# Optimization experiments

Measured on AMD Instinct MI355X. Metric: run time of the kernel, lower is better.

Reference implementation:

```python
import jax, jax.numpy as jnp
import numpy as np

B = 8
N_GENES = 19836
D_IN = 11
D_H = 64
DEG = 16
N = B * N_GENES
E_PER = N_GENES * DEG


def setup_inputs() -> dict:
    key = jax.random.key(0)
    ks = jax.random.split(key, 20)
    x = jax.random.normal(ks[0], (B, N_GENES, D_IN), dtype=jnp.float32)
    # edges: random within each graph, offset by graph index
    base_src = jax.random.randint(ks[1], (B, E_PER), 0, N_GENES)
    base_dst = jax.random.randint(ks[2], (B, E_PER), 0, N_GENES)
    offs = (jnp.arange(B) * N_GENES)[:, None]
    src = (base_src + offs).reshape(-1).astype(jnp.int64) if False else (base_src + offs).reshape(-1)
    dst = (base_dst + offs).reshape(-1)
    s = 0.02
    def nrm(k, shape):
        return jax.random.normal(k, shape, dtype=jnp.float32) * s
    return {
        'x': x, 'src': src, 'dst': dst,
        'enc_W': nrm(ks[3], (D_H, D_IN)), 'enc_b': jnp.zeros((D_H,), jnp.float32),
        'gene_emb': nrm(ks[4], (N_GENES, D_H)),
        'gin_W': nrm(ks[5], (D_H, D_H)),
        'bn_w': 1.0 + nrm(ks[6], (D_H,)), 'bn_b': jnp.zeros((D_H,), jnp.float32),
        'key_W': nrm(ks[7], (D_H, D_H)), 'key_b': jnp.zeros((D_H,), jnp.float32),
        'query_w': nrm(ks[8], (1, D_H)),
        'val_W': nrm(ks[9], (D_H, D_H)), 'val_b': jnp.zeros((D_H,), jnp.float32),
        'sae_enc_W': nrm(ks[10], (D_H, D_H)), 'sae_enc_b': jnp.zeros((D_H,), jnp.float32),
        'sae_dec_W': nrm(ks[11], (D_H, D_H)), 'sae_dec_b': jnp.zeros((D_H,), jnp.float32),
        'pred_W1': nrm(ks[12], (D_H, D_H)), 'pred_b1': jnp.zeros((D_H,), jnp.float32),
        'pred_W2': nrm(ks[13], (1, D_H)), 'pred_b2': jnp.zeros((1,), jnp.float32),
    }


def gelu(x):
    return jax.nn.gelu(x, approximate=False)  # nn.GELU default = exact erf


def batchnorm(h, w, b, eps=1e-5):
    # training-mode BatchNorm1d: batch statistics, biased variance
    mu = jnp.mean(h, axis=0)
    var = jnp.mean((h - mu) ** 2, axis=0)
    return (h - mu) * jax.lax.rsqrt(var + eps) * w + b


def reference(x, src, dst, enc_W, enc_b, gene_emb, gin_W, bn_w, bn_b,
              key_W, key_b, query_w, val_W, val_b,
              sae_enc_W, sae_enc_b, sae_dec_W, sae_dec_b,
              pred_W1, pred_b1, pred_W2, pred_b2):
    bsz, n_gene, d_in = x.shape
    n_nodes = bsz * n_gene
    # gene encoder: single Linear (bias) + GELU (inner batchnorm result is discarded in source)
    h = gelu(x.reshape(-1, d_in) @ enc_W.T + enc_b)          # [N, D_H]
    h = (h.reshape(bsz, n_gene, -1) + gene_emb).reshape(n_nodes, -1)
    # GIN layer (eps=0, sum aggregation): MLP(h + sum_{u->v} h_u); MLP = single Linear, no bias
    agg = jax.ops.segment_sum(h[src], dst, num_segments=n_nodes)  # irregular gather/scatter
    h = (h + agg) @ gin_W.T
    h = gelu(batchnorm(h, bn_w, bn_b))
    # attentive readout with SAE
    keys = h @ key_W.T + key_b
    w = jax.nn.sigmoid(keys @ query_w.T)                     # [N, 1]
    v = h @ val_W.T + val_b
    z = v * w
    enc = jax.nn.relu(z @ sae_enc_W.T + sae_enc_b)
    dec = enc @ sae_dec_W.T + sae_dec_b
    sae_loss = jnp.mean((dec - z) ** 2) + 1.0 * jnp.mean(jnp.abs(enc))
    gid = jnp.arange(n_nodes) // n_gene
    g_h = jax.ops.segment_sum(dec * w, gid, num_segments=bsz)  # [B, D_H]
    # predictor: Linear+GELU, Linear (inner batchnorm discarded in source)
    preds = gelu(g_h @ pred_W1.T + pred_b1) @ pred_W2.T + pred_b2
    return preds, w, sae_loss, dec
```

## Files before the change

kernel.cpp:

```cpp
#include <hip/hip_runtime.h>
#include <math.h>

#define NGENES 19836
#define BATCH 8
#define DIN 11
#define DH 64
#define NNODES (BATCH * NGENES)
#define NEDGES (NNODES * 16)
#define NDH (NNODES * DH)
#define NWAVE ((NNODES + 63) / 64)
#define NBLK_NODE ((NWAVE + 3) / 4)

#define SCAN_CHUNK 1024
#define NSBLK ((NNODES + SCAN_CHUNK - 1) / SCAN_CHUNK)

#define OUT_PREDS 0
#define OUT_W 8
#define OUT_SAE (8 + NNODES)
#define OUT_DEC (9 + NNODES)

__device__ __forceinline__ float gelu_f(float x) {
    return 0.5f * x * (1.0f + erff(x * 0.70710678118654752f));
}

__device__ __forceinline__ float bcast(float v, int lane) {
    return __int_as_float(__builtin_amdgcn_readlane(__float_as_int(v), lane));
}

__device__ __forceinline__ float wave_sum(float v) {
    #pragma unroll
    for (int o = 32; o; o >>= 1) v += __shfl_xor(v, o, 64);
    return v;
}

__global__ void k_encoder(const float* __restrict__ x, const float* __restrict__ encW,
                          const float* __restrict__ encB, const float* __restrict__ gemb,
                          float* __restrict__ h) {
    int lane = threadIdx.x & 63;
    int wid = (blockIdx.x * blockDim.x + threadIdx.x) >> 6;
    int tw = (gridDim.x * blockDim.x) >> 6;
    int chunk = (NNODES + tw - 1) / tw;
    int start = wid * chunk;
    int end = min(start + chunk, NNODES);
    float wreg[DIN];
    #pragma unroll
    for (int k = 0; k < DIN; ++k) wreg[k] = encW[lane * DIN + k];
    float bias = encB[lane];
    for (int node = start; node < end; ++node) {
        const float* xr = x + (size_t)node * DIN;
        float acc = bias;
        #pragma unroll
        for (int k = 0; k < DIN; ++k) acc = fmaf(xr[k], wreg[k], acc);
        int gene = node % NGENES;
        h[(size_t)node * DH + lane] = gelu_f(acc) + gemb[(size_t)gene * DH + lane];
    }
}

__global__ void k_hist(const int* __restrict__ dst, int* __restrict__ counts) {
    int i = blockIdx.x * blockDim.x + threadIdx.x;
    int stride = gridDim.x * blockDim.x;
    for (int e = i; e < NEDGES; e += stride)
        atomicAdd(&counts[dst[e]], 1);
}

__global__ void k_scan1(const int* __restrict__ counts, int* __restrict__ bsum) {
    __shared__ int red[256];
    int base = blockIdx.x * SCAN_CHUNK + threadIdx.x * 4;
    int s = 0;
    #pragma unroll
    for (int i = 0; i < 4; ++i) {
        int n = base + i;
        if (n < NNODES) s += counts[n];
    }
    red[threadIdx.x] = s;
    __syncthreads();
    for (int o = 128; o; o >>= 1) {
        if (threadIdx.x < o) red[threadIdx.x] += red[threadIdx.x + o];
        __syncthreads();
    }
    if (threadIdx.x == 0) bsum[blockIdx.x] = red[0];
}

__global__ void k_scan2(const int* __restrict__ bsum, int* __restrict__ boff) {
    __shared__ int red[256];
    int t = threadIdx.x;
    int v = (t < NSBLK) ? bsum[t] : 0;
    red[t] = v;
    __syncthreads();
    for (int o = 1; o < 256; o <<= 1) {
        int u = (t >= o) ? red[t - o] : 0;
        __syncthreads();
        red[t] += u;
        __syncthreads();
    }
    if (t < NSBLK) boff[t] = red[t] - v;
}

__global__ void k_scan3(const int* __restrict__ counts, const int* __restrict__ boff,
                        int* __restrict__ offsets, int* __restrict__ cursor) {
    __shared__ int red[256];
    int t = threadIdx.x;
    int base = blockIdx.x * SCAN_CHUNK + t * 4;
    int c[4];
    int s = 0;
    #pragma unroll
    for (int i = 0; i < 4; ++i) {
        int n = base + i;
        c[i] = (n < NNODES) ? counts[n] : 0;
        s += c[i];
    }
    red[t] = s;
    __syncthreads();
    for (int o = 1; o < 256; o <<= 1) {
        int v = (t >= o) ? red[t - o] : 0;
        __syncthreads();
        red[t] += v;
        __syncthreads();
    }
    int excl = red[t] - s + boff[blockIdx.x];
    #pragma unroll
    for (int i = 0; i < 4; ++i) {
        int n = base + i;
        if (n < NNODES) { offsets[n] = excl; cursor[n] = excl; }
        excl += c[i];
    }
}

__global__ void k_scatter(const int* __restrict__ src, const int* __restrict__ dst,
                          int* __restrict__ cursor, unsigned short* __restrict__ csr) {
    int i = blockIdx.x * blockDim.x + threadIdx.x;
    int stride = gridDim.x * blockDim.x;
    for (int e = i; e < NEDGES; e += stride) {
        int p = atomicAdd(&cursor[dst[e]], 1);
        csr[p] = (unsigned short)(src[e] % NGENES);
    }
}

__global__ void __launch_bounds__(256, 3)
k_aggin(const float* __restrict__ h, const int* __restrict__ offsets,
        const int* __restrict__ counts, const unsigned short* __restrict__ csr,
        const float* __restrict__ ginW, float* __restrict__ h2,
        float* __restrict__ stats) {
    int lane = threadIdx.x & 63;
    int wid = (blockIdx.x * blockDim.x + threadIdx.x) >> 6;
    int tw = (gridDim.x * blockDim.x) >> 6;
    float wr[DH];
    #pragma unroll
    for (int k = 0; k < DH; ++k) wr[k] = ginW[lane * DH + k];
    float s1 = 0.f, s2 = 0.f;
    for (int node = wid; node < NNODES; node += tw) {
        int gbase = (node / NGENES) * NGENES;
        float a[8];
        a[0] = h[(size_t)node * DH + lane];
        #pragma unroll
        for (int i = 1; i < 8; ++i) a[i] = 0.f;
        int start = offsets[node];
        int cnt = counts[node];
        for (int e0 = 0; e0 < cnt; e0 += 64) {
            int nn = min(64, cnt - e0);
            int iv = (lane < nn) ? (int)csr[start + e0 + lane] : 0;
            int j = 0;
            for (; j + 7 < nn; j += 8) {
                #pragma unroll
                for (int u = 0; u < 8; ++u) {
                    int v = gbase + __shfl(iv, j + u, 64);
                    a[u] += h[(size_t)v * DH + lane];
                }
            }
            for (; j < nn; ++j)
                a[0] += h[(size_t)(gbase + __shfl(iv, j, 64)) * DH + lane];
        }
        float tval = ((a[0] + a[1]) + (a[2] + a[3])) + ((a[4] + a[5]) + (a[6] + a[7]));
        float m0 = 0.f, m1 = 0.f, m2 = 0.f, m3 = 0.f;
        #pragma unroll
        for (int k = 0; k < DH; k += 4) {
            m0 = fmaf(wr[k], bcast(tval, k), m0);
            m1 = fmaf(wr[k + 1], bcast(tval, k + 1), m1);
            m2 = fmaf(wr[k + 2], bcast(tval, k + 2), m2);
            m3 = fmaf(wr[k + 3], bcast(tval, k + 3), m3);
        }
        float outv = (m0 + m1) + (m2 + m3);
        h2[(size_t)node * DH + lane] = outv;
        s1 += outv;
        s2 += outv * outv;
    }
    __shared__ float red[2][256];
    red[0][threadIdx.x] = s1;
    red[1][threadIdx.x] = s2;
    __syncthreads();
    if (threadIdx.x < 64) {
        float t1 = red[0][threadIdx.x] + red[0][threadIdx.x + 64] + red[0][threadIdx.x + 128] + red[0][threadIdx.x + 192];
        float t2 = red[1][threadIdx.x] + red[1][threadIdx.x + 64] + red[1][threadIdx.x + 128] + red[1][threadIdx.x + 192];
        atomicAdd(&stats[threadIdx.x], t1);
        atomicAdd(&stats[64 + threadIdx.x], t2);
    }
}

__global__ void k_bnparams(const float* __restrict__ stats, const float* __restrict__ bnw,
                           const float* __restrict__ bnb, const float* __restrict__ keyW,
                           const float* __restrict__ keyB, const float* __restrict__ qw,
                           float* __restrict__ bnp) {
    int d = threadIdx.x;
    float inv_n = 1.0f / (float)NNODES;
    float mu = stats[d] * inv_n;
    float var = stats[64 + d] * inv_n - mu * mu;
    float sc = bnw[d] * rsqrtf(var + 1e-5f);
    bnp[d] = sc;
    bnp[64 + d] = bnb[d] - mu * sc;
    float kq0 = 0.f, kq1 = 0.f;
    #pragma unroll
    for (int j = 0; j < DH; j += 2) {
        kq0 = fmaf(qw[j], keyW[j * DH + d], kq0);
        kq1 = fmaf(qw[j + 1], keyW[(j + 1) * DH + d], kq1);
    }
    bnp[128 + d] = kq0 + kq1;
    float qb = wave_sum(qw[d] * keyB[d]);
    if (d == 0) bnp[192] = qb;
}

__global__ void __launch_bounds__(256, 2)
k_attn(float* __restrict__ h2, const float* __restrict__ bnp,
       const float* __restrict__ valW, const float* __restrict__ valB,
       float* __restrict__ wout) {
    int lane = threadIdx.x & 63;
    int wv = (blockIdx.x * blockDim.x + threadIdx.x) >> 6;
    int node = wv * 64 + lane;
    if (node >= NNODES) return;
    float* row = h2 + (size_t)node * DH;
    float h3[DH];
    #pragma unroll
    for (int j = 0; j < 16; ++j) {
        float4 v = *reinterpret_cast<const float4*>(row + j * 4);
        h3[j * 4] = v.x; h3[j * 4 + 1] = v.y; h3[j * 4 + 2] = v.z; h3[j * 4 + 3] = v.w;
    }
    float p = bnp[192];
    #pragma unroll
    for (int k = 0; k < DH; ++k) {
        h3[k] = gelu_f(fmaf(h3[k], bnp[k], bnp[64 + k]));
        p = fmaf(h3[k], bnp[128 + k], p);
    }
    float wq = 1.0f / (1.0f + expf(-p));
    wout[node] = wq;
    #pragma unroll 1
    for (int d4 = 0; d4 < DH; d4 += 4) {
        float a0 = valB[d4], a1 = valB[d4 + 1], a2 = valB[d4 + 2], a3 = valB[d4 + 3];
        #pragma unroll
        for (int k = 0; k < DH; ++k) {
            a0 = fmaf(valW[(d4 + 0) * DH + k], h3[k], a0);
            a1 = fmaf(valW[(d4 + 1) * DH + k], h3[k], a1);
            a2 = fmaf(valW[(d4 + 2) * DH + k], h3[k], a2);
            a3 = fmaf(valW[(d4 + 3) * DH + k], h3[k], a3);
        }
        float4 v = { a0 * wq, a1 * wq, a2 * wq, a3 * wq };
        *reinterpret_cast<float4*>(row + d4) = v;
    }
}

__global__ void __launch_bounds__(256, 2)
k_saenc(const float* __restrict__ zbuf, const float* __restrict__ encW,
        const float* __restrict__ encB, float* __restrict__ encout,
        float* __restrict__ loss) {
    int lane = threadIdx.x & 63;
    int wv = (blockIdx.x * blockDim.x + threadIdx.x) >> 6;
    int node = wv * 64 + lane;
    bool act = node < NNODES;
    const float* zr = zbuf + (size_t)node * DH;
    float z[DH];
    if (act) {
        #pragma unroll
        for (int j = 0; j < 16; ++j) {
            float4 v = *reinterpret_cast<const float4*>(zr + j * 4);
            z[j * 4] = v.x; z[j * 4 + 1] = v.y; z[j * 4 + 2] = v.z; z[j * 4 + 3] = v.w;
        }
    } else {
        #pragma unroll
        for (int k = 0; k < DH; ++k) z[k] = 0.f;
    }
    float l1 = 0.f;
    float* er = encout + (size_t)node * DH;
    #pragma unroll 1
    for (int d4 = 0; d4 < DH; d4 += 4) {
        float a0 = encB[d4], a1 = encB[d4 + 1], a2 = encB[d4 + 2], a3 = encB[d4 + 3];
        #pragma unroll
        for (int k = 0; k < DH; ++k) {
            a0 = fmaf(encW[(d4 + 0) * DH + k], z[k], a0);
            a1 = fmaf(encW[(d4 + 1) * DH + k], z[k], a1);
            a2 = fmaf(encW[(d4 + 2) * DH + k], z[k], a2);
            a3 = fmaf(encW[(d4 + 3) * DH + k], z[k], a3);
        }
        a0 = fmaxf(a0, 0.f); a1 = fmaxf(a1, 0.f);
        a2 = fmaxf(a2, 0.f); a3 = fmaxf(a3, 0.f);
        l1 += (a0 + a1) + (a2 + a3);
        if (act) {
            float4 v = { a0, a1, a2, a3 };
            *reinterpret_cast<float4*>(er + d4) = v;
        }
    }
    if (!act) l1 = 0.f;
    l1 = wave_sum(l1);
    if (lane == 0) atomicAdd(&loss[1], l1);
}

__global__ void __launch_bounds__(256, 2)
k_saedec(const float* __restrict__ zbuf, const float* __restrict__ decW,
         const float* __restrict__ decB, float* __restrict__ decout,
         float* __restrict__ loss) {
    int lane = threadIdx.x & 63;
    int wv = (blockIdx.x * blockDim.x + threadIdx.x) >> 6;
    int node = wv * 64 + lane;
    bool act = node < NNODES;
    float* dr = decout + (size_t)node * DH;
    const float* zr = zbuf + (size_t)node * DH;
    float enc[DH];
    if (act) {
        #pragma unroll
        for (int j = 0; j < 16; ++j) {
            float4 v = *reinterpret_cast<const float4*>(dr + j * 4);
            enc[j * 4] = v.x; enc[j * 4 + 1] = v.y; enc[j * 4 + 2] = v.z; enc[j * 4 + 3] = v.w;
        }
    } else {
        #pragma unroll
        for (int k = 0; k < DH; ++k) enc[k] = 0.f;
    }
    float sq = 0.f;
    #pragma unroll 1
    for (int d4 = 0; d4 < DH; d4 += 4) {
        float a0 = decB[d4], a1 = decB[d4 + 1], a2 = decB[d4 + 2], a3 = decB[d4 + 3];
        #pragma unroll
        for (int k = 0; k < DH; ++k) {
            a0 = fmaf(decW[(d4 + 0) * DH + k], enc[k], a0);
            a1 = fmaf(decW[(d4 + 1) * DH + k], enc[k], a1);
            a2 = fmaf(decW[(d4 + 2) * DH + k], enc[k], a2);
            a3 = fmaf(decW[(d4 + 3) * DH + k], enc[k], a3);
        }
        if (act) {
            float4 zv = *reinterpret_cast<const float4*>(zr + d4);
            float d0 = a0 - zv.x, d1 = a1 - zv.y, d2 = a2 - zv.z, d3 = a3 - zv.w;
            sq += (d0 * d0 + d1 * d1) + (d2 * d2 + d3 * d3);
            float4 v = { a0, a1, a2, a3 };
            *reinterpret_cast<float4*>(dr + d4) = v;
        }
    }
    sq = wave_sum(sq);
    if (lane == 0) atomicAdd(&loss[0], sq);
}

__global__ void k_ghsum(const float* __restrict__ dec, const float* __restrict__ wout,
                        float* __restrict__ g_h) {
    int lane = threadIdx.x & 63;
    int wid = (blockIdx.x * blockDim.x + threadIdx.x) >> 6;
    int tw = (gridDim.x * blockDim.x) >> 6;
    int chunk = (NNODES + tw - 1) / tw;
    int gs = wid * chunk;
    int ge = min(gs + chunk, NNODES);
    if (gs >= ge) return;
    float gacc = 0.f;
    int cur_g = gs / NGENES;
    for (int n = gs; n < ge; ++n) {
        int g = n / NGENES;
        if (g != cur_g) {
            atomicAdd(&g_h[cur_g * DH + lane], gacc);
            gacc = 0.f;
            cur_g = g;
        }
        gacc = fmaf(dec[(size_t)n * DH + lane], wout[n], gacc);
    }
    atomicAdd(&g_h[cur_g * DH + lane], gacc);
}

__global__ void k_pred(const float* __restrict__ g_h, const float* __restrict__ W1,
                       const float* __restrict__ b1, const float* __restrict__ W2,
                       const float* __restrict__ b2, const float* __restrict__ loss,
                       float* __restrict__ out) {
    int lane = threadIdx.x;
    float w1[DH];
    #pragma unroll
    for (int k = 0; k < DH; ++k) w1[k] = W1[lane * DH + k];
    float bb = b1[lane], w2 = W2[lane];
    for (int g = 0; g < BATCH; ++g) {
        float gh = g_h[g * DH + lane];
        float a0 = 0.f, a1 = 0.f;
        #pragma unroll
        for (int k = 0; k < DH; k += 2) {
            a0 = fmaf(w1[k], bcast(gh, k), a0);
            a1 = fmaf(w1[k + 1], bcast(gh, k + 1), a1);
        }
        float t = gelu_f(a0 + a1 + bb);
        float p = wave_sum(t * w2);
        if (lane == 0) out[OUT_PREDS + g] = p + b2[0];
    }
    if (lane == 0) out[OUT_SAE] = (loss[0] + loss[1]) * (1.0f / ((float)NNODES * (float)DH));
}

extern "C" void kernel_launch(void* const* d_in, const int* in_sizes, int n_in,
                              void* d_out, int out_size, void* d_ws, size_t ws_size,
                              hipStream_t stream) {
    const float* x    = (const float*)d_in[0];
    const int* src    = (const int*)d_in[1];
    const int* dst    = (const int*)d_in[2];
    const float* encW = (const float*)d_in[3];
    const float* encB = (const float*)d_in[4];
    const float* gemb = (const float*)d_in[5];
    const float* ginW = (const float*)d_in[6];
    const float* bnw  = (const float*)d_in[7];
    const float* bnb  = (const float*)d_in[8];
    const float* keyW = (const float*)d_in[9];
    const float* keyB = (const float*)d_in[10];
    const float* qw   = (const float*)d_in[11];
    const float* valW = (const float*)d_in[12];
    const float* valB = (const float*)d_in[13];
    const float* saeEncW = (const float*)d_in[14];
    const float* saeEncB = (const float*)d_in[15];
    const float* saeDecW = (const float*)d_in[16];
    const float* saeDecB = (const float*)d_in[17];
    const float* pW1  = (const float*)d_in[18];
    const float* pb1  = (const float*)d_in[19];
    const float* pW2  = (const float*)d_in[20];
    const float* pb2  = (const float*)d_in[21];

    float* out = (float*)d_out;
    float* ws = (float*)d_ws;

    int*   counts  = (int*)ws;
    float* stats   = ws + NNODES;
    float* g_h     = stats + 128;
    float* loss    = g_h + 512;
    float* bnp     = loss + 2;
    int*   offsets = (int*)(bnp + 256);
    int*   cursor  = offsets + NNODES;
    unsigned short* csr = (unsigned short*)(cursor + NNODES);
    int*   bsum    = (int*)(csr + NEDGES);
    int*   boff    = bsum + 256;
    float* h2      = (float*)(boff + 256);

    float* h    = out + OUT_DEC;
    float* wout = out + OUT_W;

    hipMemsetAsync(d_ws, 0, (size_t)(NNODES + 642) * sizeof(float), stream);

    k_encoder<<<2048, 256, 0, stream>>>(x, encW, encB, gemb, h);
    k_hist<<<2048, 256, 0, stream>>>(dst, counts);
    k_scan1<<<NSBLK, 256, 0, stream>>>(counts, bsum);
    k_scan2<<<1, 256, 0, stream>>>(bsum, boff);
    k_scan3<<<NSBLK, 256, 0, stream>>>(counts, boff, offsets, cursor);
    k_scatter<<<2048, 256, 0, stream>>>(src, dst, cursor, csr);
    k_aggin<<<2048, 256, 0, stream>>>(h, offsets, counts, csr, ginW, h2, stats);
    k_bnparams<<<1, 64, 0, stream>>>(stats, bnw, bnb, keyW, keyB, qw, bnp);
    k_attn<<<NBLK_NODE, 256, 0, stream>>>(h2, bnp, valW, valB, wout);
    k_saenc<<<NBLK_NODE, 256, 0, stream>>>(h2, saeEncW, saeEncB, h, loss);
    k_saedec<<<NBLK_NODE, 256, 0, stream>>>(h2, saeDecW, saeDecB, h, loss);
    k_ghsum<<<512, 256, 0, stream>>>(h, wout, g_h);
    k_pred<<<1, 64, 0, stream>>>(g_h, pW1, pb1, pW2, pb2, loss, out);
}
```

Baseline: 991.8 us.

## Store encoder features in bf16 and map blocks per graph for locality

The encoder now writes node features in bf16, which halves the bytes the GIN aggregation gathers per neighbor. Encoder, histogram, scatter and aggregation kernels interleave blocks across the 8 graphs so that concurrently running blocks touch one graph's nodes, which should improve L2 locality for the random gathers. The GIN weight is moved from per-lane registers to LDS, and occupancy is raised from 3 to 4 blocks per CU. The bf16 storage adds rounding error in the aggregated sums, which affects accuracy.

```diff
diff --git a/kernel.cpp b/kernel.cpp
--- a/kernel.cpp
+++ b/kernel.cpp
@@ -1,4 +1,5 @@
 #include <hip/hip_runtime.h>
+#include <hip/hip_bf16.h>
 #include <math.h>
 
 #define NGENES 19836
@@ -6,6 +7,7 @@
 #define DIN 11
 #define DH 64
 #define NNODES (BATCH * NGENES)
+#define E_PER (NGENES * 16)
 #define NEDGES (NNODES * 16)
 #define NDH (NNODES * DH)
 #define NWAVE ((NNODES + 63) / 64)
@@ -35,32 +37,34 @@
 
 __global__ void k_encoder(const float* __restrict__ x, const float* __restrict__ encW,
                           const float* __restrict__ encB, const float* __restrict__ gemb,
-                          float* __restrict__ h) {
-    int lane = threadIdx.x & 63;
-    int wid = (blockIdx.x * blockDim.x + threadIdx.x) >> 6;
-    int tw = (gridDim.x * blockDim.x) >> 6;
-    int chunk = (NNODES + tw - 1) / tw;
-    int start = wid * chunk;
-    int end = min(start + chunk, NNODES);
+                          __hip_bfloat16* __restrict__ h16) {
+    int lane = threadIdx.x & 63;
+    int g = blockIdx.x & 7;
+    int wix = (blockIdx.x >> 3) * (blockDim.x >> 6) + (threadIdx.x >> 6);
+    int wper = (gridDim.x >> 3) * (blockDim.x >> 6);
     float wreg[DIN];
     #pragma unroll
     for (int k = 0; k < DIN; ++k) wreg[k] = encW[lane * DIN + k];
     float bias = encB[lane];
-    for (int node = start; node < end; ++node) {
-        const float* xr = x + (size_t)node * DIN;
+    size_t gb = (size_t)g * NGENES;
+    for (int i = wix; i < NGENES; i += wper) {
+        size_t node = gb + i;
+        const float* xr = x + node * DIN;
         float acc = bias;
         #pragma unroll
         for (int k = 0; k < DIN; ++k) acc = fmaf(xr[k], wreg[k], acc);
-        int gene = node % NGENES;
-        h[(size_t)node * DH + lane] = gelu_f(acc) + gemb[(size_t)gene * DH + lane];
+        float hv = gelu_f(acc) + gemb[(size_t)i * DH + lane];
+        h16[node * DH + lane] = __float2bfloat16(hv);
     }
 }
 
 __global__ void k_hist(const int* __restrict__ dst, int* __restrict__ counts) {
-    int i = blockIdx.x * blockDim.x + threadIdx.x;
-    int stride = gridDim.x * blockDim.x;
-    for (int e = i; e < NEDGES; e += stride)
-        atomicAdd(&counts[dst[e]], 1);
+    int g = blockIdx.x & 7;
+    int t = (blockIdx.x >> 3) * blockDim.x + threadIdx.x;
+    int nt = (gridDim.x >> 3) * blockDim.x;
+    const int* dg = dst + (size_t)g * E_PER;
+    for (int e = t; e < E_PER; e += nt)
+        atomicAdd(&counts[dg[e]], 1);
 }
 
 __global__ void k_scan1(const int* __restrict__ counts, int* __restrict__ bsum) {
@@ -128,32 +132,42 @@
 
 __global__ void k_scatter(const int* __restrict__ src, const int* __restrict__ dst,
                           int* __restrict__ cursor, unsigned short* __restrict__ csr) {
-    int i = blockIdx.x * blockDim.x + threadIdx.x;
-    int stride = gridDim.x * blockDim.x;
-    for (int e = i; e < NEDGES; e += stride) {
-        int p = atomicAdd(&cursor[dst[e]], 1);
-        csr[p] = (unsigned short)(src[e] % NGENES);
-    }
-}
-
-__global__ void __launch_bounds__(256, 3)
-k_aggin(const float* __restrict__ h, const int* __restrict__ offsets,
+    int g = blockIdx.x & 7;
+    int t = (blockIdx.x >> 3) * blockDim.x + threadIdx.x;
+    int nt = (gridDim.x >> 3) * blockDim.x;
+    const int* sg = src + (size_t)g * E_PER;
+    const int* dg = dst + (size_t)g * E_PER;
+    int gbase = g * NGENES;
+    for (int e = t; e < E_PER; e += nt) {
+        int p = atomicAdd(&cursor[dg[e]], 1);
+        csr[p] = (unsigned short)(sg[e] - gbase);
+    }
+}
+
+__global__ void __launch_bounds__(256, 4)
+k_aggin(const __hip_bfloat16* __restrict__ h16, const int* __restrict__ offsets,
         const int* __restrict__ counts, const unsigned short* __restrict__ csr,
         const float* __restrict__ ginW, float* __restrict__ h2,
         float* __restrict__ stats) {
-    int lane = threadIdx.x & 63;
-    int wid = (blockIdx.x * blockDim.x + threadIdx.x) >> 6;
-    int tw = (gridDim.x * blockDim.x) >> 6;
-    float wr[DH];
-    #pragma unroll
-    for (int k = 0; k < DH; ++k) wr[k] = ginW[lane * DH + k];
+    __shared__ float ldsW[DH * DH];
+    __shared__ float red[2][256];
+    for (int idx = threadIdx.x; idx < DH * DH; idx += 256) {
+        int k = idx >> 6, d = idx & 63;
+        ldsW[idx] = ginW[d * DH + k];
+    }
+    __syncthreads();
+    int lane = threadIdx.x & 63;
+    int g = blockIdx.x & 7;
+    int wix = (blockIdx.x >> 3) * 4 + (threadIdx.x >> 6);
+    int wper = (gridDim.x >> 3) * 4;
+    int gbase = g * NGENES;
     float s1 = 0.f, s2 = 0.f;
-    for (int node = wid; node < NNODES; node += tw) {
-        int gbase = (node / NGENES) * NGENES;
+    for (int i = wix; i < NGENES; i += wper) {
+        int node = gbase + i;
         float a[8];
-        a[0] = h[(size_t)node * DH + lane];
-        #pragma unroll
-        for (int i = 1; i < 8; ++i) a[i] = 0.f;
+        a[0] = __bfloat162float(h16[(size_t)node * DH + lane]);
+        #pragma unroll
+        for (int u = 1; u < 8; ++u) a[u] = 0.f;
         int start = offsets[node];
         int cnt = counts[node];
         for (int e0 = 0; e0 < cnt; e0 += 64) {
@@ -164,27 +178,26 @@
                 #pragma unroll
                 for (int u = 0; u < 8; ++u) {
                     int v = gbase + __shfl(iv, j + u, 64);
-                    a[u] += h[(size_t)v * DH + lane];
+                    a[u] += __bfloat162float(h16[(size_t)v * DH + lane]);
                 }
             }
             for (; j < nn; ++j)
-                a[0] += h[(size_t)(gbase + __shfl(iv, j, 64)) * DH + lane];
+                a[0] += __bfloat162float(h16[(size_t)(gbase + __shfl(iv, j, 64)) * DH + lane]);
         }
         float tval = ((a[0] + a[1]) + (a[2] + a[3])) + ((a[4] + a[5]) + (a[6] + a[7]));
         float m0 = 0.f, m1 = 0.f, m2 = 0.f, m3 = 0.f;
         #pragma unroll
         for (int k = 0; k < DH; k += 4) {
-            m0 = fmaf(wr[k], bcast(tval, k), m0);
-            m1 = fmaf(wr[k + 1], bcast(tval, k + 1), m1);
-            m2 = fmaf(wr[k + 2], bcast(tval, k + 2), m2);
-            m3 = fmaf(wr[k + 3], bcast(tval, k + 3), m3);
+            m0 = fmaf(ldsW[(k + 0) * DH + lane], bcast(tval, k + 0), m0);
+            m1 = fmaf(ldsW[(k + 1) * DH + lane], bcast(tval, k + 1), m1);
+            m2 = fmaf(ldsW[(k + 2) * DH + lane], bcast(tval, k + 2), m2);
+            m3 = fmaf(ldsW[(k + 3) * DH + lane], bcast(tval, k + 3), m3);
         }
         float outv = (m0 + m1) + (m2 + m3);
         h2[(size_t)node * DH + lane] = outv;
         s1 += outv;
         s2 += outv * outv;
     }
-    __shared__ float red[2][256];
     red[0][threadIdx.x] = s1;
     red[1][threadIdx.x] = s2;
     __syncthreads();
@@ -433,22 +446,23 @@
     int*   boff    = bsum + 256;
     float* h2      = (float*)(boff + 256);
 
-    float* h    = out + OUT_DEC;
+    __hip_bfloat16* h16 = (__hip_bfloat16*)(out + OUT_DEC);
+    float* decregion = out + OUT_DEC;
     float* wout = out + OUT_W;
 
     hipMemsetAsync(d_ws, 0, (size_t)(NNODES + 642) * sizeof(float), stream);
 
-    k_encoder<<<2048, 256, 0, stream>>>(x, encW, encB, gemb, h);
+    k_encoder<<<2048, 256, 0, stream>>>(x, encW, encB, gemb, h16);
     k_hist<<<2048, 256, 0, stream>>>(dst, counts);
     k_scan1<<<NSBLK, 256, 0, stream>>>(counts, bsum);
     k_scan2<<<1, 256, 0, stream>>>(bsum, boff);
     k_scan3<<<NSBLK, 256, 0, stream>>>(counts, boff, offsets, cursor);
     k_scatter<<<2048, 256, 0, stream>>>(src, dst, cursor, csr);
-    k_aggin<<<2048, 256, 0, stream>>>(h, offsets, counts, csr, ginW, h2, stats);
+    k_aggin<<<2048, 256, 0, stream>>>(h16, offsets, counts, csr, ginW, h2, stats);
     k_bnparams<<<1, 64, 0, stream>>>(stats, bnw, bnb, keyW, keyB, qw, bnp);
     k_attn<<<NBLK_NODE, 256, 0, stream>>>(h2, bnp, valW, valB, wout);
-    k_saenc<<<NBLK_NODE, 256, 0, stream>>>(h2, saeEncW, saeEncB, h, loss);
-    k_saedec<<<NBLK_NODE, 256, 0, stream>>>(h2, saeDecW, saeDecB, h, loss);
-    k_ghsum<<<512, 256, 0, stream>>>(h, wout, g_h);
+    k_saenc<<<NBLK_NODE, 256, 0, stream>>>(h2, saeEncW, saeEncB, decregion, loss);
+    k_saedec<<<NBLK_NODE, 256, 0, stream>>>(h2, saeDecW, saeDecB, decregion, loss);
+    k_ghsum<<<512, 256, 0, stream>>>(decregion, wout, g_h);
     k_pred<<<1, 64, 0, stream>>>(g_h, pW1, pb1, pW2, pb2, loss, out);
 }
```

After: 812.3 us. -18.1%, faster.
